# Kernel tuning notes

Measured on AMD Instinct MI355X. Metric: run time of the kernel, lower is better.

Reference implementation:

```python
import jax, jax.numpy as jnp
import numpy as np

# Dimensions: B point clouds of S points each, C channels, H heads of dim D
B, S, C, H, D = 8, 2048, 128, 4, 32
EPS = 1e-5  # GroupNorm eps (torch default)


def setup_inputs() -> dict:
    key = jax.random.key(0)
    ks = jax.random.split(key, 3)
    x = jax.random.normal(ks[0], (B, S, C), dtype=jnp.float32)
    # GroupNorm(num_groups=1) affine params (per-channel)
    gamma = jnp.ones((C,), dtype=jnp.float32)
    beta = jnp.zeros((C,), dtype=jnp.float32)
    # to_qkv: 1x1 Minkowski conv == linear, no bias; output = 3*H*D channels
    w_qkv = jax.random.normal(ks[1], (3 * H * D, C), dtype=jnp.float32) * 0.02
    # to_out: 1x1 conv with bias, H*D -> C
    w_out = jax.random.normal(ks[2], (C, H * D), dtype=jnp.float32) * 0.02
    b_out = jnp.zeros((C,), dtype=jnp.float32)
    return {"x": x, "gamma": gamma, "beta": beta, "w_qkv": w_qkv,
            "w_out": w_out, "b_out": b_out}


def reference(x, gamma, beta, w_qkv, w_out, b_out):
    scale = D ** -0.5
    # GroupNorm(num_groups=1) applied per cloud over ALL channels and points
    mu = jnp.mean(x, axis=(1, 2), keepdims=True)
    var = jnp.var(x, axis=(1, 2), keepdims=True)
    nx = (x - mu) * jax.lax.rsqrt(var + EPS) * gamma + beta  # [B,S,C]
    # Pointwise qkv projection (no bias)
    qkv = jnp.einsum('bsc,fc->bsf', nx, w_qkv)  # [B,S,3*H*D]
    q, k, v = jnp.split(qkv, 3, axis=-1)
    q = q.reshape(B, S, H, D) * scale
    k = k.reshape(B, S, H, D)
    v = v.reshape(B, S, H, D)
    # Per-cloud multi-head self-attention (block-diagonal over clouds)
    attn = jax.nn.softmax(jnp.einsum('bihd,bjhd->bhij', q, k), axis=-1)  # [B,H,S,S]
    o = jnp.einsum('bhij,bjhd->bihd', attn, v).reshape(B, S, H * D)
    # Output projection (with bias) + residual
    return jnp.einsum('bsf,cf->bsc', o, w_out) + b_out + x
```

## Files before the change

### kernel.cpp

```cpp
#include <hip/hip_runtime.h>
#include <hip/hip_bf16.h>

#define B_ 8
#define S_ 2048
#define C_ 128
#define H_ 4
#define D_ 32
#define SC_ (S_*C_)
#define HD_ (H_*D_)

typedef short bf16x8 __attribute__((ext_vector_type(8)));
typedef float f32x4 __attribute__((ext_vector_type(4)));
union FragU { uint4 u; bf16x8 h; };

__device__ __forceinline__ unsigned short f2bf(float f) {
  __hip_bfloat16 h = __float2bfloat16(f);
  return *reinterpret_cast<unsigned short*>(&h);
}
__device__ __forceinline__ unsigned int pk2(float a, float b) {
  return (unsigned int)f2bf(a) | ((unsigned int)f2bf(b) << 16);
}

__global__ __launch_bounds__(256) void k_stats1(const float* __restrict__ x,
                                                const float* __restrict__ wqkv,
                                                const float* __restrict__ wout,
                                                float* __restrict__ part,
                                                unsigned short* __restrict__ wq_bf,
                                                unsigned short* __restrict__ wo_bf) {
  __shared__ float ssum[256], ssq[256];
  int b = blockIdx.x >> 5, sl = blockIdx.x & 31;
  int tid = threadIdx.x;
  int gid = blockIdx.x * 256 + tid;
  if (gid < 16384) {
    int e = gid * 4;
    const float4 u = (e < 49152) ? *(const float4*)(wqkv + e) : *(const float4*)(wout + e - 49152);
    unsigned short tv[4] = {f2bf(u.x), f2bf(u.y), f2bf(u.z), f2bf(u.w)};
    unsigned short* dst = (e < 49152) ? (wq_bf + e) : (wo_bf + e - 49152);
    *(uint2*)dst = *(uint2*)tv;
  }
  const float4* xp = (const float4*)(x + (size_t)b * SC_);
  float sum = 0.f, sq = 0.f;
  for (int i = sl * 2048 + tid; i < (sl + 1) * 2048; i += 256) {
    float4 u = xp[i];
    sum += u.x + u.y + u.z + u.w;
    sq  += u.x*u.x + u.y*u.y + u.z*u.z + u.w*u.w;
  }
  ssum[tid] = sum; ssq[tid] = sq;
  __syncthreads();
  for (int s = 128; s > 0; s >>= 1) {
    if (tid < s) { ssum[tid] += ssum[tid + s]; ssq[tid] += ssq[tid + s]; }
    __syncthreads();
  }
  if (tid == 0) { part[blockIdx.x * 2] = ssum[0]; part[blockIdx.x * 2 + 1] = ssq[0]; }
}

__global__ __launch_bounds__(512) void k_qkv(const float* __restrict__ x,
                                             const float* __restrict__ gamma,
                                             const float* __restrict__ beta,
                                             const unsigned short* __restrict__ wq_bf,
                                             const float* __restrict__ part,
                                             unsigned short* __restrict__ q_ws,
                                             unsigned short* __restrict__ k_ws,
                                             unsigned short* __restrict__ v_ws) {
  __shared__ __align__(16) unsigned short Nls[32][136];
  __shared__ float gs[128], bs[128];
  __shared__ float st2[2];
  const int tid = threadIdx.x;
  const int w = tid >> 6, l = tid & 63, g = l >> 4, i = l & 15;
  const int gr0 = blockIdx.x * 32;
  const int b = gr0 >> 11;
  if (tid < 128) { gs[tid] = gamma[tid]; bs[tid] = beta[tid]; }
  if (tid < 32) {
    float s1 = part[(b * 32 + tid) * 2];
    float s2 = part[(b * 32 + tid) * 2 + 1];
    #pragma unroll
    for (int m = 16; m >= 1; m >>= 1) { s1 += __shfl_xor(s1, m); s2 += __shfl_xor(s2, m); }
    if (tid == 0) {
      float mu = s1 / (float)SC_;
      float var = s2 / (float)SC_ - mu * mu;
      st2[0] = mu; st2[1] = rsqrtf(var + 1e-5f);
    }
  }
  __syncthreads();
  const float mu = st2[0], rstd = st2[1];
  {
    const float4* xp = (const float4*)(x + (size_t)gr0 * C_);
    #pragma unroll
    for (int t = 0; t < 2; ++t) {
      int e = tid + t * 512;
      float4 u = xp[e];
      int r = e >> 5, c0 = (e & 31) * 4;
      float4 gv = *(const float4*)&gs[c0];
      float4 bv = *(const float4*)&bs[c0];
      unsigned short tv[4] = {
        f2bf((u.x - mu) * rstd * gv.x + bv.x),
        f2bf((u.y - mu) * rstd * gv.y + bv.y),
        f2bf((u.z - mu) * rstd * gv.z + bv.z),
        f2bf((u.w - mu) * rstd * gv.w + bv.w)};
      *(uint2*)&Nls[r][c0] = *(uint2*)tv;
    }
  }
  __syncthreads();
  f32x4 acc[2][3];
  #pragma unroll
  for (int rt = 0; rt < 2; ++rt)
    #pragma unroll
    for (int n = 0; n < 3; ++n) acc[rt][n] = (f32x4){0.f,0.f,0.f,0.f};

  #pragma unroll
  for (int kk = 0; kk < 4; ++kk) {
    FragU bfr[3];
    #pragma unroll
    for (int n = 0; n < 3; ++n)
      bfr[n].u = *(const uint4*)(wq_bf + (size_t)((w * 3 + n) * 16 + i) * 128 + kk * 32 + 8 * g);
    FragU af[2];
    #pragma unroll
    for (int rt = 0; rt < 2; ++rt) af[rt].u = *(const uint4*)&Nls[rt * 16 + i][kk * 32 + 8 * g];
    #pragma unroll
    for (int n = 0; n < 3; ++n)
      #pragma unroll
      for (int rt = 0; rt < 2; ++rt)
        acc[rt][n] = __builtin_amdgcn_mfma_f32_16x16x32_bf16(af[rt].h, bfr[n].h, acc[rt][n], 0, 0, 0);
  }
  const float SCQ = 0.17677669529663687f * 1.4426950408889634f;
  const int base64 = ((blockIdx.x & 63) >> 1) * 64;
  const int odd32 = (blockIdx.x & 1) * 32;
  #pragma unroll
  for (int n = 0; n < 3; ++n) {
    int f = (w * 3 + n) * 16 + i;
    int which = f >> 7, fi = f & 127, h = fi >> 5, dd = fi & 31;
    #pragma unroll
    for (int rt = 0; rt < 2; ++rt) {
      #pragma unroll
      for (int r = 0; r < 4; ++r) {
        int s = (gr0 + rt * 16 + 4 * g + r) & (S_ - 1);
        if (which == 0) {
          q_ws[(((size_t)b * H_ + h) * S_ + s) * D_ + dd] = f2bf(acc[rt][n][r] * SCQ);
        } else if (which == 1) {
          k_ws[(((size_t)b * H_ + h) * S_ + s) * D_ + dd] = f2bf(acc[rt][n][r]);
        } else {
          int slot = odd32 + 8 * g + 4 * rt + r;
          v_ws[(((size_t)b * H_ + h) * D_ + dd) * S_ + base64 + slot] = f2bf(acc[rt][n][r]);
        }
      }
    }
  }
}

__global__ __launch_bounds__(256) void k_attn(const unsigned short* __restrict__ qg,
                                              const unsigned short* __restrict__ kg,
                                              const unsigned short* __restrict__ vg,
                                              unsigned short* __restrict__ og) {
  __shared__ __align__(16) unsigned short Kls[2][64][40];
  __shared__ __align__(16) unsigned short Vt[2][32][72];
  const int tid = threadIdx.x;
  const int w = tid >> 6, l = tid & 63;
  const int g = l >> 4, i = l & 15;
  const int qb = blockIdx.x, h = blockIdx.y, b = blockIdx.z;
  const size_t base = ((size_t)b * H_ + h) * (size_t)(S_ * D_);

  FragU qf;
  qf.u = *(const uint4*)(qg + base + (size_t)(qb * 64 + w * 16 + i) * D_ + 8 * g);
  FragU onef;
  onef.u = (uint4){0x3F803F80u, 0x3F803F80u, 0x3F803F80u, 0x3F803F80u};

  const int sr  = tid >> 2;
  const int sc4 = tid & 3;
  const int vr  = tid >> 3;
  const int vc  = tid & 7;
  const uint4* kp = (const uint4*)(kg + base);
  const unsigned short* vt = vg + base;

  f32x4 oac[2] = {{0.f,0.f,0.f,0.f},{0.f,0.f,0.f,0.f}};
  f32x4 sac = {0.f,0.f,0.f,0.f};

  *(uint4*)&Kls[0][sr][sc4 * 8] = kp[sr * 4 + sc4];
  *(uint4*)&Vt[0][vr][vc * 8] = *(const uint4*)(vt + (size_t)vr * S_ + vc * 8);

  for (int kt = 0; kt < 32; ++kt) {
    const int cur = kt & 1;
    __syncthreads();
    uint4 nk, nv;
    if (kt < 31) {
      nk = kp[((kt + 1) * 64 + sr) * 4 + sc4];
      nv = *(const uint4*)(vt + (size_t)vr * S_ + (kt + 1) * 64 + vc * 8);
    }
    f32x4 sf[4];
    #pragma unroll
    for (int n = 0; n < 4; ++n) {
      FragU kf; kf.u = *(const uint4*)&Kls[cur][n * 16 + i][8 * g];
      f32x4 z = {0.f, 0.f, 0.f, 0.f};
      sf[n] = __builtin_amdgcn_mfma_f32_16x16x32_bf16(kf.h, qf.h, z, 0, 0, 0);
    }
    FragU pa0, pa1;
    pa0.u = (uint4){pk2(__builtin_amdgcn_exp2f(sf[0][0]), __builtin_amdgcn_exp2f(sf[0][1])),
                    pk2(__builtin_amdgcn_exp2f(sf[0][2]), __builtin_amdgcn_exp2f(sf[0][3])),
                    pk2(__builtin_amdgcn_exp2f(sf[1][0]), __builtin_amdgcn_exp2f(sf[1][1])),
                    pk2(__builtin_amdgcn_exp2f(sf[1][2]), __builtin_amdgcn_exp2f(sf[1][3]))};
    pa1.u = (uint4){pk2(__builtin_amdgcn_exp2f(sf[2][0]), __builtin_amdgcn_exp2f(sf[2][1])),
                    pk2(__builtin_amdgcn_exp2f(sf[2][2]), __builtin_amdgcn_exp2f(sf[2][3])),
                    pk2(__builtin_amdgcn_exp2f(sf[3][0]), __builtin_amdgcn_exp2f(sf[3][1])),
                    pk2(__builtin_amdgcn_exp2f(sf[3][2]), __builtin_amdgcn_exp2f(sf[3][3]))};
    sac = __builtin_amdgcn_mfma_f32_16x16x32_bf16(pa0.h, onef.h, sac, 0, 0, 0);
    #pragma unroll
    for (int n = 0; n < 2; ++n) {
      FragU vf; vf.u = *(const uint4*)&Vt[cur][n * 16 + i][8 * g];
      oac[n] = __builtin_amdgcn_mfma_f32_16x16x32_bf16(pa0.h, vf.h, oac[n], 0, 0, 0);
    }
    sac = __builtin_amdgcn_mfma_f32_16x16x32_bf16(pa1.h, onef.h, sac, 0, 0, 0);
    #pragma unroll
    for (int n = 0; n < 2; ++n) {
      FragU vf; vf.u = *(const uint4*)&Vt[cur][n * 16 + i][32 + 8 * g];
      oac[n] = __builtin_amdgcn_mfma_f32_16x16x32_bf16(pa1.h, vf.h, oac[n], 0, 0, 0);
    }
    if (kt < 31) {
      *(uint4*)&Kls[cur ^ 1][sr][sc4 * 8] = nk;
      *(uint4*)&Vt[cur ^ 1][vr][vc * 8] = nv;
    }
  }
  #pragma unroll
  for (int n = 0; n < 2; ++n) {
    #pragma unroll
    for (int r = 0; r < 4; ++r) {
      size_t row = (size_t)qb * 64 + w * 16 + 4 * g + r;
      og[((size_t)b * S_ + row) * HD_ + h * D_ + n * 16 + i] = f2bf(oac[n][r] / sac[r]);
    }
  }
}

__global__ __launch_bounds__(512) void k_out(const unsigned short* __restrict__ o,
                                             const unsigned short* __restrict__ wo_bf,
                                             const float* __restrict__ bo,
                                             const float* __restrict__ x,
                                             float* __restrict__ out) {
  const int tid = threadIdx.x;
  const int w = tid >> 6, l = tid & 63, g = l >> 4, i = l & 15;
  const int gr0 = blockIdx.x * 32;
  const int c = w * 16 + i;
  f32x4 acc[2] = {{0,0,0,0},{0,0,0,0}};
  #pragma unroll
  for (int kk = 0; kk < 4; ++kk) {
    FragU bfr;
    bfr.u = *(const uint4*)(wo_bf + (size_t)c * HD_ + kk * 32 + 8 * g);
    #pragma unroll
    for (int rt = 0; rt < 2; ++rt) {
      FragU af;
      af.u = *(const uint4*)(o + (size_t)(gr0 + rt * 16 + i) * HD_ + kk * 32 + 8 * g);
      acc[rt] = __builtin_amdgcn_mfma_f32_16x16x32_bf16(af.h, bfr.h, acc[rt], 0, 0, 0);
    }
  }
  float bias = bo[c];
  #pragma unroll
  for (int rt = 0; rt < 2; ++rt) {
    #pragma unroll
    for (int r = 0; r < 4; ++r) {
      size_t idx = (size_t)(gr0 + rt * 16 + 4 * g + r) * C_ + c;
      out[idx] = acc[rt][r] + bias + x[idx];
    }
  }
}

extern "C" void kernel_launch(void* const* d_in, const int* in_sizes, int n_in,
                              void* d_out, int out_size, void* d_ws, size_t ws_size,
                              hipStream_t stream) {
  const float* x     = (const float*)d_in[0];
  const float* gamma = (const float*)d_in[1];
  const float* beta  = (const float*)d_in[2];
  const float* wqkv  = (const float*)d_in[3];
  const float* wout  = (const float*)d_in[4];
  const float* bout  = (const float*)d_in[5];
  float* out = (float*)d_out;

  float* part  = (float*)((char*)d_ws + 64);
  unsigned short* wq_bf = (unsigned short*)((char*)d_ws + 4096);
  unsigned short* wo_bf = wq_bf + 49152;
  unsigned short* q_ws = (unsigned short*)((char*)d_ws + 4096 + 98304 + 32768);
  const size_t per = (size_t)B_ * H_ * S_ * D_;
  unsigned short* k_ws = q_ws + per;
  unsigned short* v_ws = k_ws + per;
  unsigned short* o_ws = v_ws + per;

  hipLaunchKernelGGL(k_stats1, dim3(256), dim3(256), 0, stream, x, wqkv, wout, part, wq_bf, wo_bf);
  hipLaunchKernelGGL(k_qkv, dim3(512), dim3(512), 0, stream,
                     x, gamma, beta, wq_bf, part, q_ws, k_ws, v_ws);
  hipLaunchKernelGGL(k_attn, dim3(S_ / 64, H_, B_), dim3(256), 0, stream,
                     q_ws, k_ws, v_ws, o_ws);
  hipLaunchKernelGGL(k_out, dim3(512), dim3(512), 0, stream,
                     o_ws, wo_bf, bout, x, out);
}
```

Measured before the change: 66.30 us.

## Process two query tiles per warp in attention to reuse K/V fragments

Each warp in the attention kernel now handles 32 query rows (two 16-row tiles) instead of 16, so a block covers 128 queries and the grid halves. The K and V fragments loaded from LDS each iteration are reused across both query tiles, which halves LDS and global K/V traffic per query and amortizes the loads and barriers. In exchange each thread holds more accumulators and there are half as many blocks (512 total), which lowers occupancy and may leave the GPU less evenly loaded.

```diff
diff --git a/kernel.cpp b/kernel.cpp
--- a/kernel.cpp
+++ b/kernel.cpp
@@ -159,8 +159,10 @@
   const int qb = blockIdx.x, h = blockIdx.y, b = blockIdx.z;
   const size_t base = ((size_t)b * H_ + h) * (size_t)(S_ * D_);
 
-  FragU qf;
-  qf.u = *(const uint4*)(qg + base + (size_t)(qb * 64 + w * 16 + i) * D_ + 8 * g);
+  FragU qf[2];
+  #pragma unroll
+  for (int qt = 0; qt < 2; ++qt)
+    qf[qt].u = *(const uint4*)(qg + base + (size_t)(qb * 128 + w * 32 + qt * 16 + i) * D_ + 8 * g);
   FragU onef;
   onef.u = (uint4){0x3F803F80u, 0x3F803F80u, 0x3F803F80u, 0x3F803F80u};
 
@@ -171,8 +173,9 @@
   const uint4* kp = (const uint4*)(kg + base);
   const unsigned short* vt = vg + base;
 
-  f32x4 oac[2] = {{0.f,0.f,0.f,0.f},{0.f,0.f,0.f,0.f}};
-  f32x4 sac = {0.f,0.f,0.f,0.f};
+  f32x4 oac[2][2] = {{{0.f,0.f,0.f,0.f},{0.f,0.f,0.f,0.f}},
+                     {{0.f,0.f,0.f,0.f},{0.f,0.f,0.f,0.f}}};
+  f32x4 sac[2] = {{0.f,0.f,0.f,0.f},{0.f,0.f,0.f,0.f}};
 
   *(uint4*)&Kls[0][sr][sc4 * 8] = kp[sr * 4 + sc4];
   *(uint4*)&Vt[0][vr][vc * 8] = *(const uint4*)(vt + (size_t)vr * S_ + vc * 8);
@@ -181,49 +184,57 @@
     const int cur = kt & 1;
     __syncthreads();
     uint4 nk, nv;
-    if (kt < 31) {
+    const bool pf = kt < 31;
+    if (pf) {
       nk = kp[((kt + 1) * 64 + sr) * 4 + sc4];
       nv = *(const uint4*)(vt + (size_t)vr * S_ + (kt + 1) * 64 + vc * 8);
     }
-    f32x4 sf[4];
-    #pragma unroll
-    for (int n = 0; n < 4; ++n) {
-      FragU kf; kf.u = *(const uint4*)&Kls[cur][n * 16 + i][8 * g];
-      f32x4 z = {0.f, 0.f, 0.f, 0.f};
-      sf[n] = __builtin_amdgcn_mfma_f32_16x16x32_bf16(kf.h, qf.h, z, 0, 0, 0);
-    }
-    FragU pa0, pa1;
-    pa0.u = (uint4){pk2(__builtin_amdgcn_exp2f(sf[0][0]), __builtin_amdgcn_exp2f(sf[0][1])),
-                    pk2(__builtin_amdgcn_exp2f(sf[0][2]), __builtin_amdgcn_exp2f(sf[0][3])),
-                    pk2(__builtin_amdgcn_exp2f(sf[1][0]), __builtin_amdgcn_exp2f(sf[1][1])),
-                    pk2(__builtin_amdgcn_exp2f(sf[1][2]), __builtin_amdgcn_exp2f(sf[1][3]))};
-    pa1.u = (uint4){pk2(__builtin_amdgcn_exp2f(sf[2][0]), __builtin_amdgcn_exp2f(sf[2][1])),
-                    pk2(__builtin_amdgcn_exp2f(sf[2][2]), __builtin_amdgcn_exp2f(sf[2][3])),
-                    pk2(__builtin_amdgcn_exp2f(sf[3][0]), __builtin_amdgcn_exp2f(sf[3][1])),
-                    pk2(__builtin_amdgcn_exp2f(sf[3][2]), __builtin_amdgcn_exp2f(sf[3][3]))};
-    sac = __builtin_amdgcn_mfma_f32_16x16x32_bf16(pa0.h, onef.h, sac, 0, 0, 0);
+    FragU kf[4], vf[4];
+    #pragma unroll
+    for (int n = 0; n < 4; ++n) kf[n].u = *(const uint4*)&Kls[cur][n * 16 + i][8 * g];
     #pragma unroll
     for (int n = 0; n < 2; ++n) {
-      FragU vf; vf.u = *(const uint4*)&Vt[cur][n * 16 + i][8 * g];
-      oac[n] = __builtin_amdgcn_mfma_f32_16x16x32_bf16(pa0.h, vf.h, oac[n], 0, 0, 0);
-    }
-    sac = __builtin_amdgcn_mfma_f32_16x16x32_bf16(pa1.h, onef.h, sac, 0, 0, 0);
-    #pragma unroll
-    for (int n = 0; n < 2; ++n) {
-      FragU vf; vf.u = *(const uint4*)&Vt[cur][n * 16 + i][32 + 8 * g];
-      oac[n] = __builtin_amdgcn_mfma_f32_16x16x32_bf16(pa1.h, vf.h, oac[n], 0, 0, 0);
-    }
-    if (kt < 31) {
+      vf[n].u     = *(const uint4*)&Vt[cur][n * 16 + i][8 * g];
+      vf[2 + n].u = *(const uint4*)&Vt[cur][n * 16 + i][32 + 8 * g];
+    }
+    #pragma unroll
+    for (int qt = 0; qt < 2; ++qt) {
+      f32x4 sf[4];
+      #pragma unroll
+      for (int n = 0; n < 4; ++n) {
+        f32x4 z = {0.f, 0.f, 0.f, 0.f};
+        sf[n] = __builtin_amdgcn_mfma_f32_16x16x32_bf16(kf[n].h, qf[qt].h, z, 0, 0, 0);
+      }
+      FragU pa0, pa1;
+      pa0.u = (uint4){pk2(__builtin_amdgcn_exp2f(sf[0][0]), __builtin_amdgcn_exp2f(sf[0][1])),
+                      pk2(__builtin_amdgcn_exp2f(sf[0][2]), __builtin_amdgcn_exp2f(sf[0][3])),
+                      pk2(__builtin_amdgcn_exp2f(sf[1][0]), __builtin_amdgcn_exp2f(sf[1][1])),
+                      pk2(__builtin_amdgcn_exp2f(sf[1][2]), __builtin_amdgcn_exp2f(sf[1][3]))};
+      pa1.u = (uint4){pk2(__builtin_amdgcn_exp2f(sf[2][0]), __builtin_amdgcn_exp2f(sf[2][1])),
+                      pk2(__builtin_amdgcn_exp2f(sf[2][2]), __builtin_amdgcn_exp2f(sf[2][3])),
+                      pk2(__builtin_amdgcn_exp2f(sf[3][0]), __builtin_amdgcn_exp2f(sf[3][1])),
+                      pk2(__builtin_amdgcn_exp2f(sf[3][2]), __builtin_amdgcn_exp2f(sf[3][3]))};
+      sac[qt] = __builtin_amdgcn_mfma_f32_16x16x32_bf16(pa0.h, onef.h, sac[qt], 0, 0, 0);
+      oac[qt][0] = __builtin_amdgcn_mfma_f32_16x16x32_bf16(pa0.h, vf[0].h, oac[qt][0], 0, 0, 0);
+      oac[qt][1] = __builtin_amdgcn_mfma_f32_16x16x32_bf16(pa0.h, vf[1].h, oac[qt][1], 0, 0, 0);
+      sac[qt] = __builtin_amdgcn_mfma_f32_16x16x32_bf16(pa1.h, onef.h, sac[qt], 0, 0, 0);
+      oac[qt][0] = __builtin_amdgcn_mfma_f32_16x16x32_bf16(pa1.h, vf[2].h, oac[qt][0], 0, 0, 0);
+      oac[qt][1] = __builtin_amdgcn_mfma_f32_16x16x32_bf16(pa1.h, vf[3].h, oac[qt][1], 0, 0, 0);
+    }
+    if (pf) {
       *(uint4*)&Kls[cur ^ 1][sr][sc4 * 8] = nk;
       *(uint4*)&Vt[cur ^ 1][vr][vc * 8] = nv;
     }
   }
   #pragma unroll
-  for (int n = 0; n < 2; ++n) {
-    #pragma unroll
-    for (int r = 0; r < 4; ++r) {
-      size_t row = (size_t)qb * 64 + w * 16 + 4 * g + r;
-      og[((size_t)b * S_ + row) * HD_ + h * D_ + n * 16 + i] = f2bf(oac[n][r] / sac[r]);
+  for (int qt = 0; qt < 2; ++qt) {
+    #pragma unroll
+    for (int n = 0; n < 2; ++n) {
+      #pragma unroll
+      for (int r = 0; r < 4; ++r) {
+        size_t row = (size_t)qb * 128 + w * 32 + qt * 16 + 4 * g + r;
+        og[((size_t)b * S_ + row) * HD_ + h * D_ + n * 16 + i] = f2bf(oac[qt][n][r] / sac[qt][r]);
+      }
     }
   }
 }
@@ -283,7 +294,7 @@
   hipLaunchKernelGGL(k_stats1, dim3(256), dim3(256), 0, stream, x, wqkv, wout, part, wq_bf, wo_bf);
   hipLaunchKernelGGL(k_qkv, dim3(512), dim3(512), 0, stream,
                      x, gamma, beta, wq_bf, part, q_ws, k_ws, v_ws);
-  hipLaunchKernelGGL(k_attn, dim3(S_ / 64, H_, B_), dim3(256), 0, stream,
+  hipLaunchKernelGGL(k_attn, dim3(S_ / 128, H_, B_), dim3(256), 0, stream,
                      q_ws, k_ws, v_ws, o_ws);
   hipLaunchKernelGGL(k_out, dim3(512), dim3(512), 0, stream,
                      o_ws, wo_bf, bout, x, out);
```

Result: no change. 66.47 us (+0.3%).
